# Optimization experiments

Hardware: AMD Instinct MI355X
Metric: run time of the kernel (lower is better)

Reference implementation:

```python
import jax, jax.numpy as jnp
import numpy as np

BETA = 0.25  # commitment_beta


def setup_inputs() -> dict:
    key = jax.random.key(0)
    k1, k2 = jax.random.split(key)
    B, C, H, W = 8, 256, 32, 32
    n_embed = 16384
    x = jax.random.normal(k1, (B, C, H, W), dtype=jnp.float32)
    # torch init: uniform_(-1/codebook_size, 1/codebook_size)
    weight = jax.random.uniform(k2, (n_embed, C), dtype=jnp.float32,
                                minval=-1.0 / n_embed, maxval=1.0 / n_embed)
    return {"x": x, "weight": weight}


def reference(x, weight):
    B, C, H, W = x.shape
    # b c h w -> b (h w) c
    xf = jnp.transpose(x, (0, 2, 3, 1)).reshape(B, H * W, C)
    flat = xf.reshape(-1, C)  # [N, C], N = B*H*W
    d = (jnp.sum(flat * flat, axis=1, keepdims=True)
         + jnp.sum(weight * weight, axis=1)[None, :]
         - 2.0 * flat @ weight.T)
    idx = jnp.argmin(d, axis=-1)          # [N]
    xq = weight[idx].reshape(B, H * W, C)  # codebook gather
    sg = jax.lax.stop_gradient
    loss = (BETA * jnp.mean((sg(xq) - xf) ** 2)
            + jnp.mean((xq - sg(xf)) ** 2))
    # straight-through estimator
    xq_st = xf + sg(xq - xf)
    # b (h w) c -> b c h w
    xq_img = jnp.transpose(xq_st.reshape(B, H, W, C), (0, 3, 1, 2))
    x_code = idx.reshape(B, H, W)
    return xq_img, loss, x_code
```

## Files before the change

### kernel.cpp

```cpp
#include <hip/hip_runtime.h>
#include <stdint.h>

#define NROW    8192
#define CDIM    256
#define NCODE   16384
#define MARGINF 1.6e-4f

typedef short short8 __attribute__((ext_vector_type(8)));
typedef float floatx4 __attribute__((ext_vector_type(4)));
typedef _Float16 half2v __attribute__((ext_vector_type(2)));

__device__ inline ushort f2bf(float f) {
    unsigned u = __builtin_bit_cast(unsigned, f);
    unsigned r = (u + 0x7fffu + ((u >> 16) & 1u)) >> 16;
    return (ushort)r;
}
__device__ inline unsigned fsort(float v) {
    unsigned u = __builtin_bit_cast(unsigned, v);
    return (u >> 31) ? ~u : (u | 0x80000000u);
}
__device__ inline unsigned pk_min(unsigned a, unsigned b) {
    half2v x = __builtin_bit_cast(half2v, a);
    half2v y = __builtin_bit_cast(half2v, b);
    half2v r;
    r[0] = x[0] < y[0] ? x[0] : y[0];
    r[1] = x[1] < y[1] ? x[1] : y[1];
    return __builtin_bit_cast(unsigned, r);
}

__device__ inline void gl_lds16(const ushort* g, ushort* lds) {
    __builtin_amdgcn_global_load_lds(
        (const __attribute__((address_space(1))) unsigned int*)(g),
        (__attribute__((address_space(3))) unsigned int*)(lds),
        16, 0, 0);
}

__global__ __launch_bounds__(256) void prep_x(const float* __restrict__ x,
                                              float* __restrict__ xf32,
                                              ushort* __restrict__ xbf) {
    __shared__ float tile[32][33];
    const int b = blockIdx.x, ht = blockIdx.y, ct = blockIdx.z;
    const int t = threadIdx.x;
    const int hw0 = ht * 32, c0 = ct * 32;
    {
        const int cc = t >> 5, hh = t & 31;
        #pragma unroll
        for (int i = 0; i < 4; ++i) {
            int cl = cc + i * 8;
            tile[cl][hh] = x[((size_t)(b * 256 + c0 + cl) << 10) + hw0 + hh];
        }
    }
    __syncthreads();
    {
        const int col = t & 31, row = t >> 5;
        #pragma unroll
        for (int i = 0; i < 4; ++i) {
            int r = row + i * 8;
            float v = tile[col][r];
            size_t o = ((size_t)(b * 1024 + hw0 + r) << 8) + c0 + col;
            xf32[o] = v;
            xbf[o] = f2bf(v);
        }
    }
}

__global__ __launch_bounds__(256) void prep_w2(const float* __restrict__ w,
                                               ushort* __restrict__ wbf,
                                               float* __restrict__ S2a) {
#pragma clang fp contract(off)
    const int gt = blockIdx.x * 256 + threadIdx.x;
    const int j = gt >> 1, h = gt & 1;
    const float* a = w + ((size_t)j << 8) + h * 128;
    ushort* orow = wbf + ((size_t)j << 8) + h * 128;
    float r8[8];
    #pragma unroll
    for (int l = 0; l < 8; ++l) { float v = a[l]; r8[l] = v * v; }
    for (int i = 8; i < 128; i += 8) {
        #pragma unroll
        for (int l = 0; l < 8; ++l) { float v = a[i + l]; r8[l] = r8[l] + v * v; }
    }
    float hs = ((r8[0] + r8[1]) + (r8[2] + r8[3])) + ((r8[4] + r8[5]) + (r8[6] + r8[7]));
    float other = __shfl_xor(hs, 1);
    if (h == 0) S2a[j] = hs + other;
    for (int i = 0; i < 128; i += 8) {
        ushort u8[8];
        #pragma unroll
        for (int l = 0; l < 8; ++l) u8[l] = f2bf(a[i + l]);
        *(ushort4*)(orow + i)     = make_ushort4(u8[0], u8[1], u8[2], u8[3]);
        *(ushort4*)(orow + i + 4) = make_ushort4(u8[4], u8[5], u8[6], u8[7]);
    }
}

__global__ __launch_bounds__(256) void gemm_min(const ushort* __restrict__ A,
                                                const ushort* __restrict__ Bm,
                                                const float* __restrict__ S2a,
                                                unsigned* __restrict__ bm32) {
    __shared__ __attribute__((aligned(16))) ushort As[8192];
    __shared__ __attribute__((aligned(16))) ushort Bs[8192];

    const int n0 = blockIdx.x * 128;
    const int j0 = blockIdx.y * 128;
    const int t  = threadIdx.x;
    const int wv = t >> 6, l = t & 63;
    const int wr = wv >> 1, wc = wv & 1;
    const int q  = l >> 4, c = l & 15;

    const int lr = l >> 3;
    const int lperm = (l & 7) ^ lr;
    const size_t gA0 = ((size_t)(n0 + wv * 32 + lr) << 8) + lperm * 8;
    const size_t gB0 = ((size_t)(j0 + wv * 32 + lr) << 8) + lperm * 8;
    const int ldsbase = wv * 4 * 512;

    floatx4 acc[4][4];
    #pragma unroll
    for (int mi = 0; mi < 4; ++mi)
        #pragma unroll
        for (int ni = 0; ni < 4; ++ni)
            acc[mi][ni] = (floatx4){0.f, 0.f, 0.f, 0.f};

    for (int kb = 0; kb < 4; ++kb) {
        if (kb) __syncthreads();
        #pragma unroll
        for (int ca = 0; ca < 4; ++ca) {
            gl_lds16(A + gA0 + ca * 2048 + kb * 64, As + ldsbase + ca * 512);
            gl_lds16(Bm + gB0 + ca * 2048 + kb * 64, Bs + ldsbase + ca * 512);
        }
        __syncthreads();
        #pragma unroll
        for (int kk = 0; kk < 2; ++kk) {
            short8 af[4], bf[4];
            #pragma unroll
            for (int mi = 0; mi < 4; ++mi) {
                int row = wr * 64 + mi * 16 + c;
                int pos = (kk * 4 + q) ^ (c & 7);
                af[mi] = *(const short8*)&As[row * 64 + pos * 8];
            }
            #pragma unroll
            for (int ni = 0; ni < 4; ++ni) {
                int row = wc * 64 + ni * 16 + c;
                int pos = (kk * 4 + q) ^ (c & 7);
                bf[ni] = *(const short8*)&Bs[row * 64 + pos * 8];
            }
            #pragma unroll
            for (int mi = 0; mi < 4; ++mi)
                #pragma unroll
                for (int ni = 0; ni < 4; ++ni)
                    acc[mi][ni] = __builtin_amdgcn_mfma_f32_16x16x32_bf16(
                        af[mi], bf[ni], acc[mi][ni], 0, 0, 0);
        }
    }

    float cn[4];
    #pragma unroll
    for (int ni = 0; ni < 4; ++ni) cn[ni] = S2a[j0 + wc * 64 + ni * 16 + c];

    #pragma unroll
    for (int mi = 0; mi < 4; ++mi) {
        #pragma unroll
        for (int r = 0; r < 4; ++r) {
            float v0 = fmaf(-2.f, acc[mi][0][r], cn[0]);
            float v1 = fmaf(-2.f, acc[mi][1][r], cn[1]);
            float v2 = fmaf(-2.f, acc[mi][2][r], cn[2]);
            float v3 = fmaf(-2.f, acc[mi][3][r], cn[3]);
            half2v p0, p1;
            p0[0] = (_Float16)v0; p0[1] = (_Float16)v1;
            p1[0] = (_Float16)v2; p1[1] = (_Float16)v3;
            unsigned u0 = __builtin_bit_cast(unsigned, p0);
            unsigned u1 = __builtin_bit_cast(unsigned, p1);
            #pragma unroll
            for (int off = 1; off <= 8; off <<= 1) {
                u0 = pk_min(u0, (unsigned)__shfl_xor((int)u0, off));
                u1 = pk_min(u1, (unsigned)__shfl_xor((int)u1, off));
            }
            if (c == 0) {
                int row = wr * 64 + mi * 16 + q * 4 + r;
                size_t base = ((size_t)(n0 + row) << 9) + blockIdx.y * 4 + wc * 2;
                bm32[base]     = u0;
                bm32[base + 1] = u1;
            }
        }
    }
}

__global__ __launch_bounds__(256) void rescore2(const unsigned* __restrict__ bm32,
                                                const float* __restrict__ xf32,
                                                const float* __restrict__ w,
                                                const float* __restrict__ S2a,
                                                int* __restrict__ idxb,
                                                float* __restrict__ xcode,
                                                float* __restrict__ loss) {
#pragma clang fp contract(off)
    __shared__ float xrow[256];
    __shared__ float red[256];
    __shared__ unsigned long long redk[256];
    __shared__ short list[1024];
    __shared__ int np_;
    __shared__ float sS1[2];
    const int n = blockIdx.x, t = threadIdx.x;
    if (n == 0 && t == 0) *loss = 0.f;
    if (t == 0) np_ = 0;
    xrow[t] = xf32[((size_t)n << 8) + t];
    const uint2 bm = *(const uint2*)(bm32 + ((size_t)n << 9) + t * 2);
    const half2v ha = __builtin_bit_cast(half2v, bm.x);
    const half2v hb = __builtin_bit_cast(half2v, bm.y);
    float v4[4] = {(float)ha[0], (float)ha[1], (float)hb[0], (float)hb[1]};
    float m = fminf(fminf(v4[0], v4[1]), fminf(v4[2], v4[3]));
    red[t] = m;
    __syncthreads();
    for (int s = 128; s > 0; s >>= 1) {
        if (t < s) red[t] = fminf(red[t], red[t + s]);
        __syncthreads();
    }
    const float thr = red[0] + MARGINF;
    #pragma unroll
    for (int i = 0; i < 4; ++i)
        if (v4[i] <= thr) { int p = atomicAdd(&np_, 1); list[p] = (short)(t * 4 + i); }
    if (t < 2) {
        const float* a = &xrow[t * 128];
        float r8[8];
        #pragma unroll
        for (int l = 0; l < 8; ++l) { float v = a[l]; r8[l] = v * v; }
        for (int i = 8; i < 128; i += 8) {
            #pragma unroll
            for (int l = 0; l < 8; ++l) { float v = a[i + l]; r8[l] = r8[l] + v * v; }
        }
        sS1[t] = ((r8[0] + r8[1]) + (r8[2] + r8[3])) + ((r8[4] + r8[5]) + (r8[6] + r8[7]));
    }
    __syncthreads();
    const int total = np_ * 16;
    const float S1n = sS1[0] + sS1[1];
    unsigned long long best = ~0ull;
    for (int it = t; it < total; it += 256) {
        const int j = (int)list[it >> 4] * 16 + (it & 15);
        const float* wr_ = w + ((size_t)j << 8);
        float g = 0.f;
        for (int k = 0; k < 256; k += 4) {
            float4 wv = *(const float4*)(wr_ + k);
            g = fmaf(xrow[k],     wv.x, g);
            g = fmaf(xrow[k + 1], wv.y, g);
            g = fmaf(xrow[k + 2], wv.z, g);
            g = fmaf(xrow[k + 3], wv.w, g);
        }
        float d = (S1n + S2a[j]) - 2.0f * g;
        unsigned long long key = ((unsigned long long)fsort(d) << 32) | (unsigned)j;
        if (key < best) best = key;
    }
    redk[t] = best;
    __syncthreads();
    for (int s = 128; s > 0; s >>= 1) {
        if (t < s) { if (redk[t + s] < redk[t]) redk[t] = redk[t + s]; }
        __syncthreads();
    }
    if (t == 0) {
        int J = (int)(redk[0] & 0xffffffffu);
        idxb[n] = J;
        xcode[n] = (float)J;
    }
}

__global__ __launch_bounds__(256) void outputs_k(const float* __restrict__ x,
                                                 const float* __restrict__ w,
                                                 const int* __restrict__ idxb,
                                                 float* __restrict__ out,
                                                 float* __restrict__ loss) {
    const int b = blockIdx.x, hq = blockIdx.y, cs = blockIdx.z;
    const int t = threadIdx.x;
    const int hw = hq * 256 + t;
    const int n = (b << 10) + hw;
    const int id = idxb[n];
    float lacc = 0.f;
    for (int ci = 0; ci < 32; ++ci) {
        const int c_ = cs * 32 + ci;
        const size_t oo = ((size_t)((b << 8) + c_) << 10) + hw;
        float wv = w[((size_t)id << 8) + c_];
        float xv = x[oo];
        out[oo] = wv;
        float d = wv - xv;
        lacc = fmaf(d, d, lacc);
    }
    #pragma unroll
    for (int off = 32; off; off >>= 1) lacc += __shfl_xor(lacc, off);
    __shared__ float part[4];
    if ((t & 63) == 0) part[t >> 6] = lacc;
    __syncthreads();
    if (t == 0) {
        float p = part[0] + part[1] + part[2] + part[3];
        atomicAdd(loss, p * (1.25f / 2097152.0f));
    }
}

extern "C" void kernel_launch(void* const* d_in, const int* in_sizes, int n_in,
                              void* d_out, int out_size, void* d_ws, size_t ws_size,
                              hipStream_t stream) {
    const float* x = (const float*)d_in[0];
    const float* w = (const float*)d_in[1];
    float* out = (float*)d_out;

    char* ws = (char*)d_ws;
    const size_t MB = 1024u * 1024u;
    ushort*   xbf   = (ushort*)  (ws);
    float*    xf32  = (float*)   (ws + 4 * MB);
    ushort*   wbf   = (ushort*)  (ws + 12 * MB);
    float*    S2a   = (float*)   (ws + 20 * MB);
    unsigned* bm32  = (unsigned*)(ws + 21 * MB);
    int*      idxb  = (int*)     (ws + 37 * MB);

    float* loss_ptr  = out + 2097152;
    float* xcode_ptr = out + 2097153;

    prep_x  <<<dim3(8, 32, 8), 256, 0, stream>>>(x, xf32, xbf);
    prep_w2 <<<dim3(128),      256, 0, stream>>>(w, wbf, S2a);
    gemm_min<<<dim3(64, 128),  256, 0, stream>>>(xbf, wbf, S2a, bm32);
    rescore2<<<dim3(8192),     256, 0, stream>>>(bm32, xf32, w, S2a, idxb,
                                                 xcode_ptr, loss_ptr);
    outputs_k<<<dim3(8, 4, 8), 256, 0, stream>>>(x, w, idxb, out, loss_ptr);
}
```

Baseline: 277.9 us.

## Transpose GEMM operands for cheaper min epilogue and fuse loss into rescore

Operands are swapped so codebook rows land on the accumulator's row axis. Each thread can then min-reduce its 4 accumulator values in registers and needs only two cross-lane shuffles instead of eight packed-half shuffle steps. The fp16 group minima are staged in LDS and written as coalesced 16-byte stores per x row, replacing scattered 4-byte stores. The commitment loss is now computed in rescore from the already-loaded x row and the chosen codeword, so outputs_k no longer reads x. The loss is zeroed with a memset, which adds a small extra stream operation.

Result: slower. 299.4 us (+7.7%).

```diff
diff --git a/kernel.cpp b/kernel.cpp
--- a/kernel.cpp
+++ b/kernel.cpp
@@ -18,14 +18,6 @@
 __device__ inline unsigned fsort(float v) {
     unsigned u = __builtin_bit_cast(unsigned, v);
     return (u >> 31) ? ~u : (u | 0x80000000u);
-}
-__device__ inline unsigned pk_min(unsigned a, unsigned b) {
-    half2v x = __builtin_bit_cast(half2v, a);
-    half2v y = __builtin_bit_cast(half2v, b);
-    half2v r;
-    r[0] = x[0] < y[0] ? x[0] : y[0];
-    r[1] = x[1] < y[1] ? x[1] : y[1];
-    return __builtin_bit_cast(unsigned, r);
 }
 
 __device__ inline void gl_lds16(const ushort* g, ushort* lds) {
@@ -91,12 +83,13 @@
     }
 }
 
-__global__ __launch_bounds__(256) void gemm_min(const ushort* __restrict__ A,
-                                                const ushort* __restrict__ Bm,
+__global__ __launch_bounds__(256) void gemm_min(const ushort* __restrict__ Wb,
+                                                const ushort* __restrict__ Xb,
                                                 const float* __restrict__ S2a,
-                                                unsigned* __restrict__ bm32) {
+                                                ushort* __restrict__ bm16) {
     __shared__ __attribute__((aligned(16))) ushort As[8192];
     __shared__ __attribute__((aligned(16))) ushort Bs[8192];
+    __shared__ __attribute__((aligned(16))) ushort stg[128 * 8];
 
     const int n0 = blockIdx.x * 128;
     const int j0 = blockIdx.y * 128;
@@ -107,9 +100,9 @@
 
     const int lr = l >> 3;
     const int lperm = (l & 7) ^ lr;
-    const size_t gA0 = ((size_t)(n0 + wv * 32 + lr) << 8) + lperm * 8;
-    const size_t gB0 = ((size_t)(j0 + wv * 32 + lr) << 8) + lperm * 8;
-    const int ldsbase = wv * 4 * 512;
+    const size_t gA0 = ((size_t)(j0 + wv * 32 + lr) << 8) + lperm * 8;
+    const size_t gB0 = ((size_t)(n0 + wv * 32 + lr) << 8) + lperm * 8;
+    const int ldsbase = wv * 2048;
 
     floatx4 acc[4][4];
     #pragma unroll
@@ -122,8 +115,8 @@
         if (kb) __syncthreads();
         #pragma unroll
         for (int ca = 0; ca < 4; ++ca) {
-            gl_lds16(A + gA0 + ca * 2048 + kb * 64, As + ldsbase + ca * 512);
-            gl_lds16(Bm + gB0 + ca * 2048 + kb * 64, Bs + ldsbase + ca * 512);
+            gl_lds16(Wb + gA0 + ca * 2048 + kb * 64, As + ldsbase + ca * 512);
+            gl_lds16(Xb + gB0 + ca * 2048 + kb * 64, Bs + ldsbase + ca * 512);
         }
         __syncthreads();
         #pragma unroll
@@ -150,35 +143,29 @@
         }
     }
 
-    float cn[4];
-    #pragma unroll
-    for (int ni = 0; ni < 4; ++ni) cn[ni] = S2a[j0 + wc * 64 + ni * 16 + c];
-
     #pragma unroll
     for (int mi = 0; mi < 4; ++mi) {
-        #pragma unroll
-        for (int r = 0; r < 4; ++r) {
-            float v0 = fmaf(-2.f, acc[mi][0][r], cn[0]);
-            float v1 = fmaf(-2.f, acc[mi][1][r], cn[1]);
-            float v2 = fmaf(-2.f, acc[mi][2][r], cn[2]);
-            float v3 = fmaf(-2.f, acc[mi][3][r], cn[3]);
-            half2v p0, p1;
-            p0[0] = (_Float16)v0; p0[1] = (_Float16)v1;
-            p1[0] = (_Float16)v2; p1[1] = (_Float16)v3;
-            unsigned u0 = __builtin_bit_cast(unsigned, p0);
-            unsigned u1 = __builtin_bit_cast(unsigned, p1);
-            #pragma unroll
-            for (int off = 1; off <= 8; off <<= 1) {
-                u0 = pk_min(u0, (unsigned)__shfl_xor((int)u0, off));
-                u1 = pk_min(u1, (unsigned)__shfl_xor((int)u1, off));
+        float4 s2 = *(const float4*)&S2a[j0 + wr * 64 + mi * 16 + (q << 2)];
+        #pragma unroll
+        for (int ni = 0; ni < 4; ++ni) {
+            float m0 = fmaf(-2.f, acc[mi][ni][0], s2.x);
+            float m1 = fmaf(-2.f, acc[mi][ni][1], s2.y);
+            float m2 = fmaf(-2.f, acc[mi][ni][2], s2.z);
+            float m3 = fmaf(-2.f, acc[mi][ni][3], s2.w);
+            float m = fminf(fminf(m0, m1), fminf(m2, m3));
+            m = fminf(m, __shfl_xor(m, 16));
+            m = fminf(m, __shfl_xor(m, 32));
+            if (q == 0) {
+                int qr = wc * 64 + ni * 16 + c;
+                stg[qr * 8 + wr * 4 + mi] =
+                    __builtin_bit_cast(ushort, (_Float16)m);
             }
-            if (c == 0) {
-                int row = wr * 64 + mi * 16 + q * 4 + r;
-                size_t base = ((size_t)(n0 + row) << 9) + blockIdx.y * 4 + wc * 2;
-                bm32[base]     = u0;
-                bm32[base + 1] = u1;
-            }
-        }
+        }
+    }
+    __syncthreads();
+    if (t < 128) {
+        uint4 v = *(const uint4*)&stg[t * 8];
+        *(uint4*)(bm16 + ((size_t)(n0 + t) << 10) + blockIdx.y * 8) = v;
     }
 }
 
@@ -197,7 +184,6 @@
     __shared__ int np_;
     __shared__ float sS1[2];
     const int n = blockIdx.x, t = threadIdx.x;
-    if (n == 0 && t == 0) *loss = 0.f;
     if (t == 0) np_ = 0;
     xrow[t] = xf32[((size_t)n << 8) + t];
     const uint2 bm = *(const uint2*)(bm32 + ((size_t)n << 9) + t * 2);
@@ -251,41 +237,36 @@
         if (t < s) { if (redk[t + s] < redk[t]) redk[t] = redk[t + s]; }
         __syncthreads();
     }
+    const int J = (int)(redk[0] & 0xffffffffu);
     if (t == 0) {
-        int J = (int)(redk[0] & 0xffffffffu);
         idxb[n] = J;
         xcode[n] = (float)J;
     }
-}
-
-__global__ __launch_bounds__(256) void outputs_k(const float* __restrict__ x,
-                                                 const float* __restrict__ w,
+    float dv = w[((size_t)J << 8) + t] - xrow[t];
+    float lacc = dv * dv;
+    #pragma unroll
+    for (int off = 32; off; off >>= 1) lacc += __shfl_xor(lacc, off);
+    if ((t & 63) == 0) red[t >> 6] = lacc;
+    __syncthreads();
+    if (t == 0) {
+        float p = (red[0] + red[1]) + (red[2] + red[3]);
+        atomicAdd(loss, p * (1.25f / 2097152.0f));
+    }
+}
+
+__global__ __launch_bounds__(256) void outputs_k(const float* __restrict__ w,
                                                  const int* __restrict__ idxb,
-                                                 float* __restrict__ out,
-                                                 float* __restrict__ loss) {
+                                                 float* __restrict__ out) {
     const int b = blockIdx.x, hq = blockIdx.y, cs = blockIdx.z;
     const int t = threadIdx.x;
     const int hw = hq * 256 + t;
     const int n = (b << 10) + hw;
     const int id = idxb[n];
-    float lacc = 0.f;
+    #pragma unroll 4
     for (int ci = 0; ci < 32; ++ci) {
         const int c_ = cs * 32 + ci;
         const size_t oo = ((size_t)((b << 8) + c_) << 10) + hw;
-        float wv = w[((size_t)id << 8) + c_];
-        float xv = x[oo];
-        out[oo] = wv;
-        float d = wv - xv;
-        lacc = fmaf(d, d, lacc);
-    }
-    #pragma unroll
-    for (int off = 32; off; off >>= 1) lacc += __shfl_xor(lacc, off);
-    __shared__ float part[4];
-    if ((t & 63) == 0) part[t >> 6] = lacc;
-    __syncthreads();
-    if (t == 0) {
-        float p = part[0] + part[1] + part[2] + part[3];
-        atomicAdd(loss, p * (1.25f / 2097152.0f));
+        out[oo] = w[((size_t)id << 8) + c_];
     }
 }
 
@@ -298,20 +279,22 @@
 
     char* ws = (char*)d_ws;
     const size_t MB = 1024u * 1024u;
-    ushort*   xbf   = (ushort*)  (ws);
-    float*    xf32  = (float*)   (ws + 4 * MB);
-    ushort*   wbf   = (ushort*)  (ws + 12 * MB);
-    float*    S2a   = (float*)   (ws + 20 * MB);
-    unsigned* bm32  = (unsigned*)(ws + 21 * MB);
-    int*      idxb  = (int*)     (ws + 37 * MB);
+    ushort* xbf   = (ushort*)(ws);
+    float*  xf32  = (float*) (ws + 4 * MB);
+    ushort* wbf   = (ushort*)(ws + 12 * MB);
+    float*  S2a   = (float*) (ws + 20 * MB);
+    ushort* bm16  = (ushort*)(ws + 21 * MB);
+    int*    idxb  = (int*)   (ws + 37 * MB);
 
     float* loss_ptr  = out + 2097152;
     float* xcode_ptr = out + 2097153;
 
+    hipMemsetAsync((void*)loss_ptr, 0, 4, stream);
+
     prep_x  <<<dim3(8, 32, 8), 256, 0, stream>>>(x, xf32, xbf);
     prep_w2 <<<dim3(128),      256, 0, stream>>>(w, wbf, S2a);
-    gemm_min<<<dim3(64, 128),  256, 0, stream>>>(xbf, wbf, S2a, bm32);
-    rescore2<<<dim3(8192),     256, 0, stream>>>(bm32, xf32, w, S2a, idxb,
-                                                 xcode_ptr, loss_ptr);
-    outputs_k<<<dim3(8, 4, 8), 256, 0, stream>>>(x, w, idxb, out, loss_ptr);
-}
+    gemm_min<<<dim3(64, 128),  256, 0, stream>>>(wbf, xbf, S2a, bm16);
+    rescore2<<<dim3(8192),     256, 0, stream>>>((const unsigned*)bm16, xf32, w,
+                                                 S2a, idxb, xcode_ptr, loss_ptr);
+    outputs_k<<<dim3(8, 4, 8), 256, 0, stream>>>(w, idxb, out);
+}
```
